# Optimization experiments

Hardware: AMD Instinct MI355X
Metric: run time of the kernel (lower is better)

The kernel has to match this reference:

```python
import jax, jax.numpy as jnp
import numpy as np

H, DH = 6, 64
D = H * DH
SQRT_DH = np.float32(np.sqrt(DH))


def _pool_norm(tok, ids):
    # masked mean pooling over tokens, then L2 normalize (Encoder.mean_pooling + normalize)
    mask = (ids > 0).astype(tok.dtype)[:, :, None]
    s = jnp.sum(tok * mask, axis=1) / jnp.clip(jnp.sum(mask, axis=1), 1e-9, None)
    return s / jnp.clip(jnp.linalg.norm(s, axis=1, keepdims=True), 1e-12, None)


def setup_inputs() -> dict:
    key = jax.random.key(0)
    ks = jax.random.split(key, 16)
    N_MSG, N_CON, L, E = 10000, 20000, 16, 128000
    s = 0.05
    eye = jnp.eye(DH, dtype=jnp.float32)
    inp = {}
    inp['tok_msg'] = jax.random.normal(ks[0], (N_MSG, L, D), jnp.float32)
    inp['tok_con'] = jax.random.normal(ks[1], (N_CON, L, D), jnp.float32)
    inp['ids_msg'] = jax.random.randint(ks[2], (N_MSG, L), 0, 100)
    inp['ids_con'] = jax.random.randint(ks[3], (N_CON, L), 0, 100)
    inp['src_cm'] = jax.random.randint(ks[4], (E,), 0, N_CON)
    inp['dst_cm'] = jax.random.randint(ks[5], (E,), 0, N_MSG)
    inp['src_mc'] = jax.random.randint(ks[6], (E,), 0, N_MSG)
    inp['dst_mc'] = jax.random.randint(ks[7], (E,), 0, N_CON)
    inp['lin_W'] = jax.random.normal(ks[8], (2, D, D), jnp.float32) * s
    inp['lin_b'] = jnp.zeros((2, D), jnp.float32)
    inp['kW'] = jax.random.normal(ks[9], (2, 2, D, D), jnp.float32) * s
    inp['kb'] = jnp.zeros((2, 2, D), jnp.float32)
    inp['qW'] = jax.random.normal(ks[10], (2, 2, D, D), jnp.float32) * s
    inp['qb'] = jnp.zeros((2, 2, D), jnp.float32)
    inp['vW'] = jax.random.normal(ks[11], (2, 2, D, D), jnp.float32) * s
    inp['vb'] = jnp.zeros((2, 2, D), jnp.float32)
    inp['aW'] = jax.random.normal(ks[12], (2, 2, D, D), jnp.float32) * s
    inp['ab'] = jnp.zeros((2, 2, D), jnp.float32)
    inp['a_rel'] = jax.random.normal(ks[13], (2, 2, H, DH, DH), jnp.float32) * s + eye
    inp['m_rel'] = jax.random.normal(ks[14], (2, 2, H, DH, DH), jnp.float32) * s + eye
    inp['p_rel'] = jnp.ones((2, 2, H), jnp.float32)
    inp['skip'] = jnp.ones((2, 2), jnp.float32)
    return inp


def _hgt_layer(xs, edges, kW, kb, qW, qb, vW, vb, aW, ab, a_rel, m_rel, p_rel, skip):
    # xs = [x_message, x_concept]; edges = ((src, dst) per edge type)
    k = [(xs[t] @ kW[t] + kb[t]).reshape(-1, H, DH) for t in (0, 1)]
    q = [(xs[t] @ qW[t] + qb[t]).reshape(-1, H, DH) for t in (0, 1)]
    v = [(xs[t] @ vW[t] + vb[t]).reshape(-1, H, DH) for t in (0, 1)]
    edge_meta = ((1, 0), (0, 1))  # edge type e -> (src_type, dst_type)
    agg = [None, None]
    for e, (s, d) in enumerate(edge_meta):
        si, di = edges[e]
        Nd = xs[d].shape[0]
        # relation-specific key/message transforms, per head: [E, H, DH]
        ke = jnp.einsum('ehd,hdf->ehf', k[s][si], a_rel[e])
        score = jnp.einsum('ehf,ehf->eh', q[d][di], ke) * p_rel[e] / SQRT_DH
        # softmax over incoming edges per destination node
        m = jax.ops.segment_max(score, di, num_segments=Nd)
        ex = jnp.exp(score - m[di])
        den = jax.ops.segment_sum(ex, di, num_segments=Nd)
        alpha = ex / den[di]
        msg = jnp.einsum('ehd,hdf->ehf', v[s][si], m_rel[e]) * alpha[:, :, None]
        agg[d] = jax.ops.segment_sum(msg, di, num_segments=Nd).reshape(Nd, D)
    out = []
    for t in (0, 1):
        o = jax.nn.gelu(agg[t], approximate=False) @ aW[t] + ab[t]
        a = jax.nn.sigmoid(skip[t])
        out.append(a * o + (1.0 - a) * xs[t])
    return out


def reference(tok_msg, tok_con, ids_msg, ids_con, src_cm, dst_cm, src_mc, dst_mc,
              lin_W, lin_b, kW, kb, qW, qb, vW, vb, aW, ab, a_rel, m_rel, p_rel, skip):
    x0 = jax.nn.relu(_pool_norm(tok_msg, ids_msg) @ lin_W[0] + lin_b[0])
    x1 = jax.nn.relu(_pool_norm(tok_con, ids_con) @ lin_W[1] + lin_b[1])
    edges = ((src_cm, dst_cm), (src_mc, dst_mc))
    xs = [x0, x1]
    for l in range(2):  # num_layers = 2 (hard-coded in MedicalEncoder)
        xs = _hgt_layer(xs, edges, kW[l], kb[l], qW[l], qb[l], vW[l], vb[l],
                        aW[l], ab[l], a_rel[l], m_rel[l], p_rel[l], skip[l])
    return xs[0]  # x_dict['message']
```

## Files before the change

### kernel.cpp

```cpp
#include <hip/hip_runtime.h>
#include <math.h>

#define H 6
#define DH 64
#define D 384
#define L 16
#define WSZ ((size_t)(D) * (D))
#define RSZ ((size_t)(H) * (DH) * (DH))

typedef __attribute__((ext_vector_type(8))) short short8;
typedef __attribute__((ext_vector_type(4))) float f32x4;

__device__ __forceinline__ float bf2f(unsigned short u) {
  union { unsigned int i; float f; } x; x.i = ((unsigned int)u) << 16; return x.f;
}
__device__ __forceinline__ unsigned short f2bf(float f) {
  unsigned int x = __float_as_uint(f);
  x = x + 0x7fffu + ((x >> 16) & 1u);
  return (unsigned short)(x >> 16);
}
__device__ __forceinline__ float geluf(float x) {
  return 0.5f * x * (1.0f + erff(x * 0.70710678118654752f));
}

__global__ void zero_int_kernel(int* p, long n) {
  long i = (long)blockIdx.x * blockDim.x + threadIdx.x;
  long stride = (long)gridDim.x * blockDim.x;
  for (; i < n; i += stride) p[i] = 0;
}

__global__ void pool_norm_kernel(const float* __restrict__ tok, const int* __restrict__ ids,
                                 unsigned short* __restrict__ out, int N) {
  int n = blockIdx.x;
  int t = threadIdx.x;
  const float* tp = tok + (size_t)n * L * D;
  const int* ip = ids + (size_t)n * L;
  float s = 0.f;
  int cnt = 0;
#pragma unroll
  for (int l = 0; l < L; ++l) {
    int m = (ip[l] > 0);
    cnt += m;
    s += tp[(size_t)l * D + t] * (float)m;
  }
  float mean = s / fmaxf((float)cnt, 1e-9f);
  float v = mean * mean;
#pragma unroll
  for (int off = 32; off; off >>= 1) v += __shfl_down(v, off);
  __shared__ float part[D / 64];
  if ((t & 63) == 0) part[t >> 6] = v;
  __syncthreads();
  float tot = 0.f;
#pragma unroll
  for (int i = 0; i < D / 64; ++i) tot += part[i];
  float inv = 1.0f / fmaxf(sqrtf(tot), 1e-12f);
  out[(size_t)n * D + t] = f2bf(mean * inv);
}

__global__ void prepw_kernel(const float* __restrict__ lin_W, const float* __restrict__ kW,
                             const float* __restrict__ qW, const float* __restrict__ vW,
                             const float* __restrict__ aW, const float* __restrict__ a_rel,
                             const float* __restrict__ m_rel, unsigned short* __restrict__ wbuf) {
  int z = blockIdx.z;
  const float* src; const float* rel = nullptr; int type = 0;
  switch (z) {
    case 0: src = lin_W; break;
    case 1: src = lin_W + WSZ; break;
    case 2: src = kW; break;
    case 3: type = 1; src = qW; rel = a_rel; break;
    case 4: type = 2; src = vW; rel = m_rel + RSZ; break;
    case 5: src = kW + WSZ; break;
    case 6: type = 1; src = qW + WSZ; rel = a_rel + RSZ; break;
    case 7: type = 2; src = vW + WSZ; rel = m_rel; break;
    case 8: type = 1; src = qW + 2 * WSZ; rel = a_rel + 2 * RSZ; break;
    case 9: src = kW + 3 * WSZ; break;
    case 10: type = 2; src = vW + 3 * WSZ; rel = m_rel + 2 * RSZ; break;
    case 11: src = aW; break;
    case 12: src = aW + WSZ; break;
    default: src = aW + 2 * WSZ; break;
  }
  unsigned short* dst = wbuf + (size_t)z * WSZ;
  int tx = threadIdx.x, ty = threadIdx.y;
  int bx = blockIdx.x * 32;
  int by = blockIdx.y * 32;
  if (type == 0) {
    __shared__ float tile[32][33];
    tile[ty][tx] = src[(size_t)(bx + ty) * D + by + tx];
    __syncthreads();
    dst[(size_t)(by + ty) * D + bx + tx] = f2bf(tile[tx][ty]);
  } else if (type == 1) {
    int h = by >> 6, d0 = by & 63;
    __shared__ float Wt_[32][65], Rt[32][65];
#pragma unroll
    for (int half = 0; half < 2; ++half) {
      Wt_[ty][tx + half * 32] = src[(size_t)(bx + ty) * D + h * 64 + tx + half * 32];
      Rt[ty][tx + half * 32] = rel[(size_t)h * 4096 + (size_t)(d0 + ty) * 64 + tx + half * 32];
    }
    __syncthreads();
    float s = 0.f;
#pragma unroll 16
    for (int f = 0; f < 64; ++f) s += Wt_[tx][f] * Rt[ty][f];
    dst[(size_t)(by + ty) * D + bx + tx] = f2bf(s);
  } else {
    int h = by >> 6, f0 = by & 63;
    __shared__ float Wt_[32][65];
    __shared__ float Mt[64][33];
#pragma unroll
    for (int half = 0; half < 2; ++half) {
      Wt_[ty][tx + half * 32] = src[(size_t)(bx + ty) * D + h * 64 + tx + half * 32];
      Mt[ty * 2 + half][tx] = rel[(size_t)h * 4096 + (size_t)(ty * 2 + half) * 64 + f0 + tx];
    }
    __syncthreads();
    float s = 0.f;
#pragma unroll 16
    for (int d = 0; d < 64; ++d) s += Wt_[tx][d] * Mt[d][ty];
    dst[(size_t)(by + ty) * D + bx + tx] = f2bf(s);
  }
}

__global__ void prepb_kernel(const float* __restrict__ kb, const float* __restrict__ qb,
                             const float* __restrict__ vb, const float* __restrict__ a_rel,
                             const float* __restrict__ m_rel, float* __restrict__ bbuf) {
  int i = blockIdx.x * 256 + threadIdx.x;
  if (i >= 3456) return;
  int gemm, col;
  if (i < 1152) { gemm = 0; col = i; }
  else if (i < 2304) { gemm = 1; col = i - 1152; }
  else if (i < 2688) { gemm = 2; col = i - 2304; }
  else { gemm = 3; col = i - 2688; }
  int sec = col / D, j = col % D, h = j >> 6, r = j & 63;
  float out = 0.f;
  if (gemm == 0) {
    if (sec == 0) out = kb[j];
    else if (sec == 1) {
      const float* R = a_rel + (size_t)h * 4096 + (size_t)r * 64;
      float s = 0.f; for (int f = 0; f < 64; ++f) s += qb[h * 64 + f] * R[f]; out = s;
    } else {
      const float* Mm = m_rel + RSZ + (size_t)h * 4096;
      float s = 0.f; for (int d = 0; d < 64; ++d) s += vb[h * 64 + d] * Mm[d * 64 + r]; out = s;
    }
  } else if (gemm == 1) {
    if (sec == 0) out = kb[D + j];
    else if (sec == 1) {
      const float* R = a_rel + RSZ + (size_t)h * 4096 + (size_t)r * 64;
      float s = 0.f; for (int f = 0; f < 64; ++f) s += qb[D + h * 64 + f] * R[f]; out = s;
    } else {
      const float* Mm = m_rel + (size_t)h * 4096;
      float s = 0.f; for (int d = 0; d < 64; ++d) s += vb[D + h * 64 + d] * Mm[d * 64 + r]; out = s;
    }
  } else if (gemm == 2) {
    const float* R = a_rel + 2 * RSZ + (size_t)h * 4096 + (size_t)r * 64;
    float s = 0.f; for (int f = 0; f < 64; ++f) s += qb[2 * D + h * 64 + f] * R[f]; out = s;
  } else {
    if (sec == 0) out = kb[3 * D + j];
    else {
      const float* Mm = m_rel + 2 * RSZ + (size_t)h * 4096;
      float s = 0.f; for (int d = 0; d < 64; ++d) s += vb[3 * D + h * 64 + d] * Mm[d * 64 + r]; out = s;
    }
  }
  bbuf[i] = out;
}

__global__ void count2_kernel(const int* __restrict__ d0, const int* __restrict__ d1,
                              int* __restrict__ deg0, int* __restrict__ deg1, int E) {
  int e = blockIdx.x * blockDim.x + threadIdx.x;
  if (e < E) atomicAdd(&deg0[d0[e]], 1);
  else if (e < 2 * E) atomicAdd(&deg1[d1[e - E]], 1);
}

__global__ void scan2_kernel(const int* __restrict__ deg0, int* __restrict__ off0, int N0,
                             const int* __restrict__ deg1, int* __restrict__ off1, int N1) {
  const int* deg = blockIdx.x ? deg1 : deg0;
  int* off = blockIdx.x ? off1 : off0;
  int N = blockIdx.x ? N1 : N0;
  __shared__ int tmp[1024];
  __shared__ int carry;
  int tid = threadIdx.x;
  if (tid == 0) carry = 0;
  __syncthreads();
  for (int base = 0; base < N; base += 1024) {
    int i = base + tid;
    int v = (i < N) ? deg[i] : 0;
    tmp[tid] = v;
    __syncthreads();
    for (int s = 1; s < 1024; s <<= 1) {
      int t2 = (tid >= s) ? tmp[tid - s] : 0;
      __syncthreads();
      tmp[tid] += t2;
      __syncthreads();
    }
    int inc = tmp[tid];
    int c = carry;
    if (i < N) off[i] = c + inc - v;
    int tot = tmp[1023];
    __syncthreads();
    if (tid == 0) carry = c + tot;
    __syncthreads();
  }
  if (tid == 0) off[N] = carry;
}

__global__ void scatter2_kernel(const int* __restrict__ d0, const int* __restrict__ s0,
                                const int* __restrict__ off0, int* __restrict__ cur0,
                                int* __restrict__ el0,
                                const int* __restrict__ d1, const int* __restrict__ s1,
                                const int* __restrict__ off1, int* __restrict__ cur1,
                                int* __restrict__ el1, int E) {
  int e = blockIdx.x * blockDim.x + threadIdx.x;
  if (e < E) {
    int d = d0[e];
    el0[off0[d] + atomicAdd(&cur0[d], 1)] = s0[e];
  } else if (e < 2 * E) {
    int ee = e - E;
    int d = d1[ee];
    el1[off1[d] + atomicAdd(&cur1[d], 1)] = s1[ee];
  }
}

__global__ void attn_kernel(const unsigned short* __restrict__ kb, int sk,
                            const unsigned short* __restrict__ tqb, int st,
                            const unsigned short* __restrict__ vmb, int sv,
                            const int* __restrict__ off, const int* __restrict__ elist,
                            const float* __restrict__ prel,
                            unsigned short* __restrict__ aggb, int N) {
  int node = blockIdx.x * 4 + (threadIdx.x >> 6);
  int lane = threadIdx.x & 63;
  if (node >= N) return;
  int e0 = off[node], e1 = off[node + 1];
  float tq[H], pr8[H], m[H], den[H], acc[H];
#pragma unroll
  for (int h = 0; h < H; ++h) {
    tq[h] = bf2f(tqb[(size_t)node * st + h * DH + lane]);
    pr8[h] = prel[h] * 0.125f;
    m[h] = -1e30f; den[h] = 0.f; acc[h] = 0.f;
  }
  int i = e0;
  for (; i + 2 <= e1; i += 2) {
    int s0 = elist[i], s1 = elist[i + 1];
    const unsigned short* k0 = kb + (size_t)s0 * sk;
    const unsigned short* k1 = kb + (size_t)s1 * sk;
    const unsigned short* v0 = vmb + (size_t)s0 * sv;
    const unsigned short* v1 = vmb + (size_t)s1 * sv;
    float sa[H], sb[H], va[H], vb[H];
#pragma unroll
    for (int h = 0; h < H; ++h) {
      sa[h] = bf2f(k0[h * DH + lane]) * tq[h];
      sb[h] = bf2f(k1[h * DH + lane]) * tq[h];
      va[h] = bf2f(v0[h * DH + lane]);
      vb[h] = bf2f(v1[h * DH + lane]);
    }
#pragma unroll
    for (int o = 32; o; o >>= 1)
#pragma unroll
      for (int h = 0; h < H; ++h) {
        sa[h] += __shfl_xor(sa[h], o);
        sb[h] += __shfl_xor(sb[h], o);
      }
#pragma unroll
    for (int h = 0; h < H; ++h) {
      float x0 = sa[h] * pr8[h], x1 = sb[h] * pr8[h];
      float mn = fmaxf(m[h], fmaxf(x0, x1));
      float r = __expf(m[h] - mn);
      float p0 = __expf(x0 - mn);
      float p1 = __expf(x1 - mn);
      den[h] = den[h] * r + p0 + p1;
      acc[h] = acc[h] * r + p0 * va[h] + p1 * vb[h];
      m[h] = mn;
    }
  }
  if (i < e1) {
    int s0 = elist[i];
    const unsigned short* k0 = kb + (size_t)s0 * sk;
    const unsigned short* v0 = vmb + (size_t)s0 * sv;
    float sa[H], va[H];
#pragma unroll
    for (int h = 0; h < H; ++h) {
      sa[h] = bf2f(k0[h * DH + lane]) * tq[h];
      va[h] = bf2f(v0[h * DH + lane]);
    }
#pragma unroll
    for (int o = 32; o; o >>= 1)
#pragma unroll
      for (int h = 0; h < H; ++h) sa[h] += __shfl_xor(sa[h], o);
#pragma unroll
    for (int h = 0; h < H; ++h) {
      float x0 = sa[h] * pr8[h];
      float mn = fmaxf(m[h], x0);
      float r = __expf(m[h] - mn);
      float p0 = __expf(x0 - mn);
      den[h] = den[h] * r + p0;
      acc[h] = acc[h] * r + p0 * va[h];
      m[h] = mn;
    }
  }
  unsigned short* op = aggb + (size_t)node * D;
#pragma unroll
  for (int h = 0; h < H; ++h) {
    float o = (e1 > e0) ? acc[h] / den[h] : 0.f;
    op[h * DH + lane] = f2bf(geluf(o));
  }
}

__global__ __launch_bounds__(512) void gemm_bf16(
    const unsigned short* __restrict__ A, const unsigned short* __restrict__ Wt,
    const float* __restrict__ bias, float* __restrict__ Cf,
    unsigned short* __restrict__ Cb, int M, int cpitch, int relu,
    const float* __restrict__ xold, const float* __restrict__ skipPtr) {
  __shared__ __align__(16) unsigned short As[2][128 * 64];
  __shared__ __align__(16) unsigned short Bs[2][128 * 64];
  const int tid = threadIdx.x;
  const int w = tid >> 6, lane = tid & 63;
  const int bm = blockIdx.x * 128, bn = blockIdx.y * 128;

  auto stageA = [&](int t, int buf) {
#pragma unroll
    for (int i = 0; i < 2; ++i) {
      int cid = (w * 2 + i) * 64 + lane;
      int row = cid >> 3;
      int cg = (cid & 7) ^ (row & 7);
      int grow = bm + row;
      if (grow >= M) grow = M - 1;
      const unsigned short* gp = A + (size_t)grow * D + t * 64 + cg * 8;
      unsigned short* lp = &As[buf][(w * 2 + i) * 512];
      __builtin_amdgcn_global_load_lds((const __attribute__((address_space(1))) void*)gp,
                                       (__attribute__((address_space(3))) void*)lp, 16, 0, 0);
    }
  };
  auto stageB = [&](int t, int buf) {
#pragma unroll
    for (int i = 0; i < 2; ++i) {
      int cid = (w * 2 + i) * 64 + lane;
      int row = cid >> 3;
      int cg = (cid & 7) ^ (row & 7);
      const unsigned short* gp = Wt + (size_t)(bn + row) * D + t * 64 + cg * 8;
      unsigned short* lp = &Bs[buf][(w * 2 + i) * 512];
      __builtin_amdgcn_global_load_lds((const __attribute__((address_space(1))) void*)gp,
                                       (__attribute__((address_space(3))) void*)lp, 16, 0, 0);
    }
  };

  stageA(0, 0);
  stageB(0, 0);
  __syncthreads();

  const int wr = w >> 2, wc = w & 3;
  const int la = lane & 15, hi = lane >> 4;
  f32x4 acc[4][2] = {};

  for (int t = 0; t < 6; ++t) {
    if (t < 5) {
      stageA(t + 1, (t + 1) & 1);
      stageB(t + 1, (t + 1) & 1);
    }
    const unsigned short* Ab = As[t & 1];
    const unsigned short* Bb = Bs[t & 1];
#pragma unroll
    for (int ks = 0; ks < 2; ++ks) {
      int c = ks * 4 + hi;
      short8 af[4], bfr[2];
#pragma unroll
      for (int mi = 0; mi < 4; ++mi) {
        int row = wr * 64 + mi * 16 + la;
        af[mi] = *(const short8*)&Ab[row * 64 + ((c ^ (row & 7)) * 8)];
      }
#pragma unroll
      for (int n = 0; n < 2; ++n) {
        int col = wc * 32 + n * 16 + la;
        bfr[n] = *(const short8*)&Bb[col * 64 + ((c ^ (col & 7)) * 8)];
      }
#pragma unroll
      for (int mi = 0; mi < 4; ++mi)
#pragma unroll
        for (int n = 0; n < 2; ++n)
          acc[mi][n] = __builtin_amdgcn_mfma_f32_16x16x32_bf16(af[mi], bfr[n], acc[mi][n], 0, 0, 0);
    }
    __syncthreads();
  }

  float sa = 0.f;
  if (xold) sa = 1.0f / (1.0f + __expf(-*skipPtr));
#pragma unroll
  for (int mi = 0; mi < 4; ++mi) {
#pragma unroll
    for (int n = 0; n < 2; ++n) {
#pragma unroll
      for (int r = 0; r < 4; ++r) {
        int row = bm + wr * 64 + mi * 16 + hi * 4 + r;
        int col = bn + wc * 32 + n * 16 + la;
        if (row >= M) continue;
        float v = acc[mi][n][r] + bias[col];
        if (relu) v = fmaxf(v, 0.f);
        if (xold) v = sa * v + (1.0f - sa) * xold[(size_t)row * D + col];
        if (Cf) Cf[(size_t)row * cpitch + col] = v;
        if (Cb) Cb[(size_t)row * cpitch + col] = f2bf(v);
      }
    }
  }
}

extern "C" void kernel_launch(void* const* d_in, const int* in_sizes, int n_in,
                              void* d_out, int out_size, void* d_ws, size_t ws_size,
                              hipStream_t stream) {
  const float* tok_msg = (const float*)d_in[0];
  const float* tok_con = (const float*)d_in[1];
  const int* ids_msg = (const int*)d_in[2];
  const int* ids_con = (const int*)d_in[3];
  const int* src_cm = (const int*)d_in[4];
  const int* dst_cm = (const int*)d_in[5];
  const int* src_mc = (const int*)d_in[6];
  const int* dst_mc = (const int*)d_in[7];
  const float* lin_W = (const float*)d_in[8];
  const float* lin_b = (const float*)d_in[9];
  const float* kW = (const float*)d_in[10];
  const float* kb = (const float*)d_in[11];
  const float* qW = (const float*)d_in[12];
  const float* qb = (const float*)d_in[13];
  const float* vW = (const float*)d_in[14];
  const float* vb = (const float*)d_in[15];
  const float* aW = (const float*)d_in[16];
  const float* ab = (const float*)d_in[17];
  const float* a_rel = (const float*)d_in[18];
  const float* m_rel = (const float*)d_in[19];
  const float* p_rel = (const float*)d_in[20];
  const float* skip = (const float*)d_in[21];

  const int NM = in_sizes[2] / L;
  const int NC = in_sizes[3] / L;
  const int E = in_sizes[4];

  char* wsb = (char*)d_ws;
  size_t woff = 0;
  auto alloc = [&](size_t bytes) {
    woff = (woff + 255) & ~(size_t)255;
    void* p = wsb + woff;
    woff += bytes;
    return p;
  };
  const size_t NMe = (size_t)NM * D, NCe = (size_t)NC * D;
  unsigned short* poolM = (unsigned short*)alloc(NMe * 2);
  unsigned short* poolC = (unsigned short*)alloc(NCe * 2);
  float* x0f = (float*)alloc(NMe * 4);
  float* x1f = (float*)alloc(NCe * 4);
  float* xn0f = (float*)alloc(NMe * 4);
  unsigned short* x0b = (unsigned short*)alloc(NMe * 2);
  unsigned short* x1b = (unsigned short*)alloc(NCe * 2);
  unsigned short* xn0b = (unsigned short*)alloc(NMe * 2);
  unsigned short* xn1b = (unsigned short*)alloc(NCe * 2);
  unsigned short* projM1 = (unsigned short*)alloc((size_t)NM * 1152 * 2);
  unsigned short* projC1 = (unsigned short*)alloc((size_t)NC * 1152 * 2);
  unsigned short* projM2 = (unsigned short*)alloc((size_t)NM * 384 * 2);
  unsigned short* projC2 = (unsigned short*)alloc((size_t)NC * 768 * 2);
  unsigned short* aggM = (unsigned short*)alloc(NMe * 2);
  unsigned short* aggC = (unsigned short*)alloc(NCe * 2);
  unsigned short* wbuf = (unsigned short*)alloc(14 * WSZ * 2);
  float* bbuf = (float*)alloc(3456 * 4);
  long nz = 2L * NM + 2L * NC;
  int* ibase = (int*)alloc((size_t)(nz + NM + 1 + NC + 1 + 2L * E) * 4);
  int* deg0 = ibase;
  int* cur0 = deg0 + NM;
  int* deg1 = cur0 + NM;
  int* cur1 = deg1 + NC;
  int* off0 = cur1 + NC;
  int* off1 = off0 + NM + 1;
  int* el0 = off1 + NC + 1;
  int* el1 = el0 + E;

  dim3 b256(256), b512(512);
  auto gg = [](int M, int N) { return dim3((M + 127) / 128, N / 128); };

  prepw_kernel<<<dim3(12, 12, 14), dim3(32, 32), 0, stream>>>(lin_W, kW, qW, vW, aW, a_rel, m_rel, wbuf);
  prepb_kernel<<<14, b256, 0, stream>>>(kb, qb, vb, a_rel, m_rel, bbuf);

  zero_int_kernel<<<64, b256, 0, stream>>>(ibase, nz);
  int eg2 = (2 * E + 255) / 256;
  count2_kernel<<<eg2, b256, 0, stream>>>(dst_cm, dst_mc, deg0, deg1, E);
  scan2_kernel<<<2, 1024, 0, stream>>>(deg0, off0, NM, deg1, off1, NC);
  scatter2_kernel<<<eg2, b256, 0, stream>>>(dst_cm, src_cm, off0, cur0, el0,
                                            dst_mc, src_mc, off1, cur1, el1, E);

  pool_norm_kernel<<<NM, D, 0, stream>>>(tok_msg, ids_msg, poolM, NM);
  pool_norm_kernel<<<NC, D, 0, stream>>>(tok_con, ids_con, poolC, NC);
  gemm_bf16<<<gg(NM, D), b512, 0, stream>>>(poolM, wbuf, lin_b, x0f, x0b, NM, D, 1, nullptr, nullptr);
  gemm_bf16<<<gg(NC, D), b512, 0, stream>>>(poolC, wbuf + WSZ, lin_b + D, x1f, x1b, NC, D, 1, nullptr, nullptr);

  gemm_bf16<<<gg(NM, 1152), b512, 0, stream>>>(x0b, wbuf + 2 * WSZ, bbuf, nullptr, projM1, NM, 1152, 0, nullptr, nullptr);
  gemm_bf16<<<gg(NC, 1152), b512, 0, stream>>>(x1b, wbuf + 5 * WSZ, bbuf + 1152, nullptr, projC1, NC, 1152, 0, nullptr, nullptr);
  attn_kernel<<<(NM + 3) / 4, b256, 0, stream>>>(projC1, 1152, projM1 + 384, 1152, projC1 + 768, 1152,
                                                 off0, el0, p_rel, aggM, NM);
  attn_kernel<<<(NC + 3) / 4, b256, 0, stream>>>(projM1, 1152, projC1 + 384, 1152, projM1 + 768, 1152,
                                                 off1, el1, p_rel + H, aggC, NC);
  gemm_bf16<<<gg(NM, D), b512, 0, stream>>>(aggM, wbuf + 11 * WSZ, ab, xn0f, xn0b, NM, D, 0, x0f, skip + 0);
  gemm_bf16<<<gg(NC, D), b512, 0, stream>>>(aggC, wbuf + 12 * WSZ, ab + D, nullptr, xn1b, NC, D, 0, x1f, skip + 1);

  gemm_bf16<<<gg(NM, D), b512, 0, stream>>>(xn0b, wbuf + 8 * WSZ, bbuf + 2304, nullptr, projM2, NM, 384, 0, nullptr, nullptr);
  gemm_bf16<<<gg(NC, 768), b512, 0, stream>>>(xn1b, wbuf + 9 * WSZ, bbuf + 2688, nullptr, projC2, NC, 768, 0, nullptr, nullptr);
  attn_kernel<<<(NM + 3) / 4, b256, 0, stream>>>(projC2, 768, projM2, 384, projC2 + 384, 768,
                                                 off0, el0, p_rel + 2 * H, aggM, NM);
  gemm_bf16<<<gg(NM, D), b512, 0, stream>>>(aggM, wbuf + 13 * WSZ, ab + 2 * D, (float*)d_out, nullptr, NM, D, 0, xn0f, skip + 2);
}
```

Baseline: 713.8 us.

## Batch paired launches, warp-shuffle scan, and retile GEMM to 256 threads

Merges the message and concept launches of pool_norm, attention and each GEMM pair into single grouped launches selected by block index, cutting launch count and tail gaps. The scan kernel switches from a shared-memory Hillis-Steele scan with many barriers to a wave-shuffle scan with per-wave sums. The GEMM changes from 512 threads with double-buffered LDS to 256 threads with a single buffer and a 4x4 MFMA tile per wave, giving up load/compute overlap in exchange for lower LDS use and more register reuse. Grouped GEMM grids are sized to the larger M, so some blocks exit early.

```diff
diff --git a/kernel.cpp b/kernel.cpp
--- a/kernel.cpp
+++ b/kernel.cpp
@@ -29,9 +29,14 @@
   for (; i < n; i += stride) p[i] = 0;
 }
 
-__global__ void pool_norm_kernel(const float* __restrict__ tok, const int* __restrict__ ids,
-                                 unsigned short* __restrict__ out, int N) {
+__global__ void pool_norm_kernel(const float* __restrict__ tokM, const int* __restrict__ idsM,
+                                 unsigned short* __restrict__ outM, int NM,
+                                 const float* __restrict__ tokC, const int* __restrict__ idsC,
+                                 unsigned short* __restrict__ outC) {
   int n = blockIdx.x;
+  const float* tok; const int* ids; unsigned short* out;
+  if (n < NM) { tok = tokM; ids = idsM; out = outM; }
+  else { n -= NM; tok = tokC; ids = idsC; out = outC; }
   int t = threadIdx.x;
   const float* tp = tok + (size_t)n * L * D;
   const int* ip = ids + (size_t)n * L;
@@ -173,31 +178,32 @@
   const int* deg = blockIdx.x ? deg1 : deg0;
   int* off = blockIdx.x ? off1 : off0;
   int N = blockIdx.x ? N1 : N0;
-  __shared__ int tmp[1024];
-  __shared__ int carry;
+  __shared__ int wsum[16];
+  __shared__ int carrySh;
   int tid = threadIdx.x;
-  if (tid == 0) carry = 0;
+  int lane = tid & 63, wid = tid >> 6;
+  if (tid == 0) carrySh = 0;
   __syncthreads();
   for (int base = 0; base < N; base += 1024) {
     int i = base + tid;
     int v = (i < N) ? deg[i] : 0;
-    tmp[tid] = v;
-    __syncthreads();
-    for (int s = 1; s < 1024; s <<= 1) {
-      int t2 = (tid >= s) ? tmp[tid - s] : 0;
-      __syncthreads();
-      tmp[tid] += t2;
-      __syncthreads();
-    }
-    int inc = tmp[tid];
-    int c = carry;
-    if (i < N) off[i] = c + inc - v;
-    int tot = tmp[1023];
-    __syncthreads();
-    if (tid == 0) carry = c + tot;
-    __syncthreads();
-  }
-  if (tid == 0) off[N] = carry;
+    int s = v;
+#pragma unroll
+    for (int o = 1; o < 64; o <<= 1) {
+      int t = __shfl_up(s, o);
+      if (lane >= o) s += t;
+    }
+    if (lane == 63) wsum[wid] = s;
+    __syncthreads();
+    int wpre = 0;
+    for (int j = 0; j < wid; ++j) wpre += wsum[j];
+    int c = carrySh;
+    if (i < N) off[i] = c + wpre + s - v;
+    __syncthreads();
+    if (tid == 1023) carrySh = c + wpre + s;
+    __syncthreads();
+  }
+  if (tid == 0) off[N] = carrySh;
 }
 
 __global__ void scatter2_kernel(const int* __restrict__ d0, const int* __restrict__ s0,
@@ -217,30 +223,39 @@
   }
 }
 
-__global__ void attn_kernel(const unsigned short* __restrict__ kb, int sk,
-                            const unsigned short* __restrict__ tqb, int st,
-                            const unsigned short* __restrict__ vmb, int sv,
-                            const int* __restrict__ off, const int* __restrict__ elist,
-                            const float* __restrict__ prel,
-                            unsigned short* __restrict__ aggb, int N) {
-  int node = blockIdx.x * 4 + (threadIdx.x >> 6);
+struct AttnP {
+  const unsigned short* kb;
+  const unsigned short* tqb;
+  const unsigned short* vmb;
+  const int* off;
+  const int* elist;
+  const float* prel;
+  unsigned short* aggb;
+  int N, sk, st, sv, nb;
+};
+
+__global__ void attn_kernel(AttnP a0, AttnP a1) {
+  bool first = (int)blockIdx.x < a0.nb;
+  AttnP a = first ? a0 : a1;
+  int bx = first ? blockIdx.x : blockIdx.x - a0.nb;
+  int node = bx * 4 + (threadIdx.x >> 6);
   int lane = threadIdx.x & 63;
-  if (node >= N) return;
-  int e0 = off[node], e1 = off[node + 1];
+  if (node >= a.N) return;
+  int e0 = a.off[node], e1 = a.off[node + 1];
   float tq[H], pr8[H], m[H], den[H], acc[H];
 #pragma unroll
   for (int h = 0; h < H; ++h) {
-    tq[h] = bf2f(tqb[(size_t)node * st + h * DH + lane]);
-    pr8[h] = prel[h] * 0.125f;
+    tq[h] = bf2f(a.tqb[(size_t)node * a.st + h * DH + lane]);
+    pr8[h] = a.prel[h] * 0.125f;
     m[h] = -1e30f; den[h] = 0.f; acc[h] = 0.f;
   }
   int i = e0;
   for (; i + 2 <= e1; i += 2) {
-    int s0 = elist[i], s1 = elist[i + 1];
-    const unsigned short* k0 = kb + (size_t)s0 * sk;
-    const unsigned short* k1 = kb + (size_t)s1 * sk;
-    const unsigned short* v0 = vmb + (size_t)s0 * sv;
-    const unsigned short* v1 = vmb + (size_t)s1 * sv;
+    int s0 = a.elist[i], s1 = a.elist[i + 1];
+    const unsigned short* k0 = a.kb + (size_t)s0 * a.sk;
+    const unsigned short* k1 = a.kb + (size_t)s1 * a.sk;
+    const unsigned short* v0 = a.vmb + (size_t)s0 * a.sv;
+    const unsigned short* v1 = a.vmb + (size_t)s1 * a.sv;
     float sa[H], sb[H], va[H], vb[H];
 #pragma unroll
     for (int h = 0; h < H; ++h) {
@@ -269,9 +284,9 @@
     }
   }
   if (i < e1) {
-    int s0 = elist[i];
-    const unsigned short* k0 = kb + (size_t)s0 * sk;
-    const unsigned short* v0 = vmb + (size_t)s0 * sv;
+    int s0 = a.elist[i];
+    const unsigned short* k0 = a.kb + (size_t)s0 * a.sk;
+    const unsigned short* v0 = a.vmb + (size_t)s0 * a.sv;
     float sa[H], va[H];
 #pragma unroll
     for (int h = 0; h < H; ++h) {
@@ -293,7 +308,7 @@
       m[h] = mn;
     }
   }
-  unsigned short* op = aggb + (size_t)node * D;
+  unsigned short* op = a.aggb + (size_t)node * D;
 #pragma unroll
   for (int h = 0; h < H; ++h) {
     float o = (e1 > e0) ? acc[h] / den[h] : 0.f;
@@ -301,98 +316,92 @@
   }
 }
 
-__global__ __launch_bounds__(512) void gemm_bf16(
-    const unsigned short* __restrict__ A, const unsigned short* __restrict__ Wt,
-    const float* __restrict__ bias, float* __restrict__ Cf,
-    unsigned short* __restrict__ Cb, int M, int cpitch, int relu,
-    const float* __restrict__ xold, const float* __restrict__ skipPtr) {
-  __shared__ __align__(16) unsigned short As[2][128 * 64];
-  __shared__ __align__(16) unsigned short Bs[2][128 * 64];
+struct GemmP {
+  const unsigned short* A;
+  const unsigned short* Wt;
+  const float* bias;
+  float* Cf;
+  unsigned short* Cb;
+  const float* xold;
+  const float* skipPtr;
+  int M, N, cpitch, relu;
+};
+
+__global__ __launch_bounds__(256) void gemm_bf16(GemmP q0, GemmP q1) {
+  GemmP p = blockIdx.z ? q1 : q0;
+  const int bm = blockIdx.x * 128, bn = blockIdx.y * 128;
+  if (bm >= p.M || bn >= p.N) return;
+  __shared__ __align__(16) unsigned short As[128 * 64];
+  __shared__ __align__(16) unsigned short Bs[128 * 64];
   const int tid = threadIdx.x;
   const int w = tid >> 6, lane = tid & 63;
-  const int bm = blockIdx.x * 128, bn = blockIdx.y * 128;
-
-  auto stageA = [&](int t, int buf) {
-#pragma unroll
-    for (int i = 0; i < 2; ++i) {
-      int cid = (w * 2 + i) * 64 + lane;
+  const int wr = w >> 1, wc = w & 1;
+  const int la = lane & 15, hi = lane >> 4;
+  f32x4 acc[4][4] = {};
+
+  for (int t = 0; t < 6; ++t) {
+#pragma unroll
+    for (int i = 0; i < 4; ++i) {
+      int cid = (w * 4 + i) * 64 + lane;
       int row = cid >> 3;
       int cg = (cid & 7) ^ (row & 7);
       int grow = bm + row;
-      if (grow >= M) grow = M - 1;
-      const unsigned short* gp = A + (size_t)grow * D + t * 64 + cg * 8;
-      unsigned short* lp = &As[buf][(w * 2 + i) * 512];
+      if (grow >= p.M) grow = p.M - 1;
+      const unsigned short* gp = p.A + (size_t)grow * D + t * 64 + cg * 8;
+      unsigned short* lp = &As[(w * 4 + i) * 512];
       __builtin_amdgcn_global_load_lds((const __attribute__((address_space(1))) void*)gp,
                                        (__attribute__((address_space(3))) void*)lp, 16, 0, 0);
     }
-  };
-  auto stageB = [&](int t, int buf) {
-#pragma unroll
-    for (int i = 0; i < 2; ++i) {
-      int cid = (w * 2 + i) * 64 + lane;
+#pragma unroll
+    for (int i = 0; i < 4; ++i) {
+      int cid = (w * 4 + i) * 64 + lane;
       int row = cid >> 3;
       int cg = (cid & 7) ^ (row & 7);
-      const unsigned short* gp = Wt + (size_t)(bn + row) * D + t * 64 + cg * 8;
-      unsigned short* lp = &Bs[buf][(w * 2 + i) * 512];
+      const unsigned short* gp = p.Wt + (size_t)(bn + row) * D + t * 64 + cg * 8;
+      unsigned short* lp = &Bs[(w * 4 + i) * 512];
       __builtin_amdgcn_global_load_lds((const __attribute__((address_space(1))) void*)gp,
                                        (__attribute__((address_space(3))) void*)lp, 16, 0, 0);
     }
-  };
-
-  stageA(0, 0);
-  stageB(0, 0);
-  __syncthreads();
-
-  const int wr = w >> 2, wc = w & 3;
-  const int la = lane & 15, hi = lane >> 4;
-  f32x4 acc[4][2] = {};
-
-  for (int t = 0; t < 6; ++t) {
-    if (t < 5) {
-      stageA(t + 1, (t + 1) & 1);
-      stageB(t + 1, (t + 1) & 1);
-    }
-    const unsigned short* Ab = As[t & 1];
-    const unsigned short* Bb = Bs[t & 1];
+    __syncthreads();
 #pragma unroll
     for (int ks = 0; ks < 2; ++ks) {
       int c = ks * 4 + hi;
-      short8 af[4], bfr[2];
+      short8 af[4], bfr[4];
 #pragma unroll
       for (int mi = 0; mi < 4; ++mi) {
         int row = wr * 64 + mi * 16 + la;
-        af[mi] = *(const short8*)&Ab[row * 64 + ((c ^ (row & 7)) * 8)];
+        af[mi] = *(const short8*)&As[row * 64 + ((c ^ (row & 7)) * 8)];
       }
 #pragma unroll
-      for (int n = 0; n < 2; ++n) {
-        int col = wc * 32 + n * 16 + la;
-        bfr[n] = *(const short8*)&Bb[col * 64 + ((c ^ (col & 7)) * 8)];
+      for (int n = 0; n < 4; ++n) {
+        int col = wc * 64 + n * 16 + la;
+        bfr[n] = *(const short8*)&Bs[col * 64 + ((c ^ (col & 7)) * 8)];
       }
 #pragma unroll
       for (int mi = 0; mi < 4; ++mi)
 #pragma unroll
-        for (int n = 0; n < 2; ++n)
+        for (int n = 0; n < 4; ++n)
           acc[mi][n] = __builtin_amdgcn_mfma_f32_16x16x32_bf16(af[mi], bfr[n], acc[mi][n], 0, 0, 0);
     }
     __syncthreads();
   }
 
   float sa = 0.f;
-  if (xold) sa = 1.0f / (1.0f + __expf(-*skipPtr));
+  if (p.xold) sa = 1.0f / (1.0f + __expf(-*p.skipPtr));
 #pragma unroll
   for (int mi = 0; mi < 4; ++mi) {
 #pragma unroll
-    for (int n = 0; n < 2; ++n) {
+    for (int n = 0; n < 4; ++n) {
 #pragma unroll
       for (int r = 0; r < 4; ++r) {
         int row = bm + wr * 64 + mi * 16 + hi * 4 + r;
-        int col = bn + wc * 32 + n * 16 + la;
-        if (row >= M) continue;
-        float v = acc[mi][n][r] + bias[col];
-        if (relu) v = fmaxf(v, 0.f);
-        if (xold) v = sa * v + (1.0f - sa) * xold[(size_t)row * D + col];
-        if (Cf) Cf[(size_t)row * cpitch + col] = v;
-        if (Cb) Cb[(size_t)row * cpitch + col] = f2bf(v);
+        int col = bn + wc * 64 + n * 16 + la;
+        if (row >= p.M) continue;
+        float v = acc[mi][n][r] + p.bias[col];
+        if (p.relu) v = fmaxf(v, 0.f);
+        if (p.xold) v = sa * v + (1.0f - sa) * p.xold[(size_t)row * D + col];
+        if (p.Cf) p.Cf[(size_t)row * p.cpitch + col] = v;
+        if (p.Cb) p.Cb[(size_t)row * p.cpitch + col] = f2bf(v);
       }
     }
   }
@@ -465,8 +474,9 @@
   int* el0 = off1 + NC + 1;
   int* el1 = el0 + E;
 
-  dim3 b256(256), b512(512);
-  auto gg = [](int M, int N) { return dim3((M + 127) / 128, N / 128); };
+  dim3 b256(256);
+  const int mbM = (NM + 127) / 128, mbC = (NC + 127) / 128;
+  const int mbMax = (mbM > mbC) ? mbM : mbC;
 
   prepw_kernel<<<dim3(12, 12, 14), dim3(32, 32), 0, stream>>>(lin_W, kW, qW, vW, aW, a_rel, m_rel, wbuf);
   prepb_kernel<<<14, b256, 0, stream>>>(kb, qb, vb, a_rel, m_rel, bbuf);
@@ -478,23 +488,41 @@
   scatter2_kernel<<<eg2, b256, 0, stream>>>(dst_cm, src_cm, off0, cur0, el0,
                                             dst_mc, src_mc, off1, cur1, el1, E);
 
-  pool_norm_kernel<<<NM, D, 0, stream>>>(tok_msg, ids_msg, poolM, NM);
-  pool_norm_kernel<<<NC, D, 0, stream>>>(tok_con, ids_con, poolC, NC);
-  gemm_bf16<<<gg(NM, D), b512, 0, stream>>>(poolM, wbuf, lin_b, x0f, x0b, NM, D, 1, nullptr, nullptr);
-  gemm_bf16<<<gg(NC, D), b512, 0, stream>>>(poolC, wbuf + WSZ, lin_b + D, x1f, x1b, NC, D, 1, nullptr, nullptr);
-
-  gemm_bf16<<<gg(NM, 1152), b512, 0, stream>>>(x0b, wbuf + 2 * WSZ, bbuf, nullptr, projM1, NM, 1152, 0, nullptr, nullptr);
-  gemm_bf16<<<gg(NC, 1152), b512, 0, stream>>>(x1b, wbuf + 5 * WSZ, bbuf + 1152, nullptr, projC1, NC, 1152, 0, nullptr, nullptr);
-  attn_kernel<<<(NM + 3) / 4, b256, 0, stream>>>(projC1, 1152, projM1 + 384, 1152, projC1 + 768, 1152,
-                                                 off0, el0, p_rel, aggM, NM);
-  attn_kernel<<<(NC + 3) / 4, b256, 0, stream>>>(projM1, 1152, projC1 + 384, 1152, projM1 + 768, 1152,
-                                                 off1, el1, p_rel + H, aggC, NC);
-  gemm_bf16<<<gg(NM, D), b512, 0, stream>>>(aggM, wbuf + 11 * WSZ, ab, xn0f, xn0b, NM, D, 0, x0f, skip + 0);
-  gemm_bf16<<<gg(NC, D), b512, 0, stream>>>(aggC, wbuf + 12 * WSZ, ab + D, nullptr, xn1b, NC, D, 0, x1f, skip + 1);
-
-  gemm_bf16<<<gg(NM, D), b512, 0, stream>>>(xn0b, wbuf + 8 * WSZ, bbuf + 2304, nullptr, projM2, NM, 384, 0, nullptr, nullptr);
-  gemm_bf16<<<gg(NC, 768), b512, 0, stream>>>(xn1b, wbuf + 9 * WSZ, bbuf + 2688, nullptr, projC2, NC, 768, 0, nullptr, nullptr);
-  attn_kernel<<<(NM + 3) / 4, b256, 0, stream>>>(projC2, 768, projM2, 384, projC2 + 384, 768,
-                                                 off0, el0, p_rel + 2 * H, aggM, NM);
-  gemm_bf16<<<gg(NM, D), b512, 0, stream>>>(aggM, wbuf + 13 * WSZ, ab + 2 * D, (float*)d_out, nullptr, NM, D, 0, xn0f, skip + 2);
-}
+  pool_norm_kernel<<<NM + NC, D, 0, stream>>>(tok_msg, ids_msg, poolM, NM, tok_con, ids_con, poolC);
+
+  {
+    GemmP p0 = {poolM, wbuf, lin_b, x0f, x0b, nullptr, nullptr, NM, D, D, 1};
+    GemmP p1 = {poolC, wbuf + WSZ, lin_b + D, x1f, x1b, nullptr, nullptr, NC, D, D, 1};
+    gemm_bf16<<<dim3(mbMax, 3, 2), b256, 0, stream>>>(p0, p1);
+  }
+  {
+    GemmP p0 = {x0b, wbuf + 2 * WSZ, bbuf, nullptr, projM1, nullptr, nullptr, NM, 1152, 1152, 0};
+    GemmP p1 = {x1b, wbuf + 5 * WSZ, bbuf + 1152, nullptr, projC1, nullptr, nullptr, NC, 1152, 1152, 0};
+    gemm_bf16<<<dim3(mbMax, 9, 2), b256, 0, stream>>>(p0, p1);
+  }
+  {
+    AttnP a0 = {projC1, projM1 + 384, projC1 + 768, off0, el0, p_rel, aggM, NM, 1152, 1152, 1152, (NM + 3) / 4};
+    AttnP a1 = {projM1, projC1 + 384, projM1 + 768, off1, el1, p_rel + H, aggC, NC, 1152, 1152, 1152, (NC + 3) / 4};
+    attn_kernel<<<(NM + 3) / 4 + (NC + 3) / 4, b256, 0, stream>>>(a0, a1);
+  }
+  {
+    GemmP p0 = {aggM, wbuf + 11 * WSZ, ab, xn0f, xn0b, x0f, skip + 0, NM, D, D, 0};
+    GemmP p1 = {aggC, wbuf + 12 * WSZ, ab + D, nullptr, xn1b, x1f, skip + 1, NC, D, D, 0};
+    gemm_bf16<<<dim3(mbMax, 3, 2), b256, 0, stream>>>(p0, p1);
+  }
+  {
+    GemmP p0 = {xn0b, wbuf + 8 * WSZ, bbuf + 2304, nullptr, projM2, nullptr, nullptr, NM, 384, 384, 0};
+    GemmP p1 = {xn1b, wbuf + 9 * WSZ, bbuf + 2688, nullptr, projC2, nullptr, nullptr, NC, 768, 768, 0};
+    gemm_bf16<<<dim3(mbMax, 6, 2), b256, 0, stream>>>(p0, p1);
+  }
+  {
+    AttnP a0 = {projC2, projM2, projC2 + 384, off0, el0, p_rel + 2 * H, aggM, NM, 768, 384, 768, (NM + 3) / 4};
+    AttnP a1 = a0;
+    attn_kernel<<<(NM + 3) / 4, b256, 0, stream>>>(a0, a1);
+  }
+  {
+    GemmP p0 = {aggM, wbuf + 13 * WSZ, ab + 2 * D, (float*)d_out, nullptr, xn0f, skip + 2, NM, D, D, 0};
+    GemmP p1 = p0;
+    gemm_bf16<<<dim3(mbM, 3, 1), b256, 0, stream>>>(p0, p1);
+  }
+}
```

Result: slower. 764.9 us (+7.2%).
